# Optimization experiments

Hardware: AMD Instinct MI355X
Metric: run time of the kernel (lower is better)

The kernel has to match this reference:

```python
import jax, jax.numpy as jnp
import numpy as np

N_HEADS = 8
D_K = 64
SCALE = D_K ** (-0.5)


def setup_inputs() -> dict:
    key = jax.random.key(0)
    k1, k2, k3 = jax.random.split(key, 3)
    B, C, H, W = 8, 512, 32, 32
    x = jax.random.normal(k1, (B, C, H, W), dtype=jnp.float32)
    # Linear weights stored as [in, out] so y = x @ W + b (same math as torch Linear)
    W_qkv = jax.random.normal(k2, (C, N_HEADS * D_K * 3), dtype=jnp.float32) * (1.0 / np.sqrt(C))
    b_qkv = jnp.zeros((N_HEADS * D_K * 3,), dtype=jnp.float32)
    W_out = jax.random.normal(k3, (N_HEADS * D_K, C), dtype=jnp.float32) * (1.0 / np.sqrt(N_HEADS * D_K))
    b_out = jnp.zeros((C,), dtype=jnp.float32)
    return {"x": x, "W_qkv": W_qkv, "b_qkv": b_qkv, "W_out": W_out, "b_out": b_out}


def reference(x, W_qkv, b_qkv, W_out, b_out):
    B, C, H, W = x.shape
    N = H * W
    # [B, C, H, W] -> [B, N, C]  (tokens are spatial positions)
    xf = jnp.transpose(x.reshape(B, C, N), (0, 2, 1))
    # NOTE: the original forward never applies self.norm, so neither do we.
    qkv = xf @ W_qkv + b_qkv                       # [B, N, 3*h*d]
    qkv = qkv.reshape(B, N, N_HEADS, 3 * D_K)
    q, k, v = jnp.split(qkv, 3, axis=-1)           # each [B, N, h, d]
    attn = jnp.einsum('bihd,bjhd->bijh', q, k) * SCALE
    attn = jax.nn.softmax(attn, axis=2)            # softmax over key index j
    res = jnp.einsum('bijh,bjhd->bihd', attn, v)   # [B, N, h, d]
    res = res.reshape(B, N, N_HEADS * D_K)
    res = res @ W_out + b_out
    res = res + xf                                 # residual
    res = jnp.transpose(res, (0, 2, 1)).reshape(B, C, H, W)
    return res
```

## Files before the change

kernel.cpp:

```cpp
#include <hip/hip_runtime.h>
#include <hip/hip_bf16.h>
#include <cstdint>

typedef __bf16 bf16;
typedef __attribute__((ext_vector_type(8))) __bf16 bf16x8;
typedef __attribute__((ext_vector_type(4))) __bf16 bf16x4;
typedef __attribute__((ext_vector_type(4))) float f32x4;

#define CEXP 0.1803368801111244f

__global__ __launch_bounds__(256) void prep_all(const float* __restrict__ x,
                                                const float* __restrict__ Wqkv,
                                                const float* __restrict__ Wout,
                                                bf16* __restrict__ xT,
                                                bf16* __restrict__ WqkvT,
                                                bf16* __restrict__ WoutT) {
  __shared__ bf16 t[32][33];
  const int z = blockIdx.z;
  const float* src;
  bf16* dst;
  int C;
  if (z < 8) {
    if (blockIdx.x >= 32) return;
    src = x + (size_t)z * 512 * 1024;
    dst = xT + (size_t)z * 1024 * 512;
    C = 1024;
  } else if (z == 8) {
    src = Wqkv; dst = WqkvT; C = 1536;
  } else {
    if (blockIdx.x >= 16) return;
    src = Wout; dst = WoutT; C = 512;
  }
  const int c0 = blockIdx.x * 32, r0 = blockIdx.y * 32;
  const int tx = threadIdx.x, ty = threadIdx.y;
#pragma unroll
  for (int i = 0; i < 4; ++i)
    t[ty + i * 8][tx] = (bf16)src[(size_t)(r0 + ty + i * 8) * C + c0 + tx];
  __syncthreads();
#pragma unroll
  for (int i = 0; i < 4; ++i)
    dst[(size_t)(c0 + ty + i * 8) * 512 + r0 + tx] = t[tx][ty + i * 8];
}

__global__ __launch_bounds__(256, 3) void gemm_qkv(const bf16* __restrict__ xT,
                                                   const bf16* __restrict__ WqkvT,
                                                   const float* __restrict__ bqkv,
                                                   bf16* __restrict__ Qb,
                                                   bf16* __restrict__ Kb,
                                                   bf16* __restrict__ Vb) {
  __shared__ bf16 As[128 * 72];
  __shared__ bf16 Bs[64 * 72];
  const int b = blockIdx.z;
  const int m0 = blockIdx.y * 128;
  const int co0 = blockIdx.x * 64;
  const int tid = threadIdx.x;
  const int w = tid >> 6, l = tid & 63;
  const int wr = w >> 1, wc = w & 1;
  const int quad = l >> 4, l16 = l & 15;

  const bf16* A = xT + (size_t)b * 1024 * 512;

  f32x4 acc[4][2];
#pragma unroll
  for (int i = 0; i < 4; ++i)
#pragma unroll
    for (int j = 0; j < 2; ++j) acc[i][j] = (f32x4){0.f, 0.f, 0.f, 0.f};

  const int srow = w * 32 + (l >> 3);
  const int scol = (l & 7) * 8;
  const int brow = tid >> 2;
  const int bcol = (tid & 3) * 16;

  for (int kk = 0; kk < 8; ++kk) {
    const int k0 = kk * 64;
    bf16x8 av[4], bv[2];
#pragma unroll
    for (int i = 0; i < 4; ++i)
      av[i] = *(const bf16x8*)&A[(size_t)(m0 + srow + i * 8) * 512 + k0 + scol];
#pragma unroll
    for (int i = 0; i < 2; ++i)
      bv[i] = *(const bf16x8*)&WqkvT[(size_t)(co0 + brow) * 512 + k0 + bcol + i * 8];
#pragma unroll
    for (int i = 0; i < 4; ++i)
      *(bf16x8*)&As[(srow + i * 8) * 72 + scol] = av[i];
#pragma unroll
    for (int i = 0; i < 2; ++i)
      *(bf16x8*)&Bs[brow * 72 + bcol + i * 8] = bv[i];
    __syncthreads();
#pragma unroll
    for (int ks = 0; ks < 2; ++ks) {
      bf16x8 a[4], bb[2];
#pragma unroll
      for (int rb = 0; rb < 4; ++rb)
        a[rb] = *(const bf16x8*)&As[(wr * 64 + rb * 16 + l16) * 72 + ks * 32 + quad * 8];
#pragma unroll
      for (int cb = 0; cb < 2; ++cb)
        bb[cb] = *(const bf16x8*)&Bs[(wc * 32 + cb * 16 + l16) * 72 + ks * 32 + quad * 8];
#pragma unroll
      for (int rb = 0; rb < 4; ++rb)
#pragma unroll
        for (int cb = 0; cb < 2; ++cb)
          acc[rb][cb] = __builtin_amdgcn_mfma_f32_16x16x32_bf16(a[rb], bb[cb], acc[rb][cb], 0, 0, 0);
    }
    __syncthreads();
  }

  const int h = co0 / 192;
  const int part = (co0 - h * 192) >> 6;
#pragma unroll
  for (int cb = 0; cb < 2; ++cb) {
    const int dd = wc * 32 + cb * 16 + l16;
    const float bias = bqkv[co0 + dd];
    if (part == 2) {
      bf16* base = Vb + ((size_t)(b * 8 + h) * 64 + dd) * 1024;
#pragma unroll
      for (int rb = 0; rb < 4; ++rb) {
        const int n = m0 + wr * 64 + rb * 16 + quad * 4;
        f32x4 v = acc[rb][cb];
        bf16x4 ov;
#pragma unroll
        for (int r = 0; r < 4; ++r) ov[r] = (bf16)(v[r] + bias);
        *(bf16x4*)&base[n] = ov;
      }
    } else {
      const float sc = (part == 0) ? CEXP : 1.0f;
      bf16* dst = (part == 0) ? Qb : Kb;
      bf16* base = dst + ((size_t)(b * 8 + h) * 1024) * 64 + dd;
#pragma unroll
      for (int rb = 0; rb < 4; ++rb) {
        const int n = m0 + wr * 64 + rb * 16 + quad * 4;
        f32x4 v = acc[rb][cb];
#pragma unroll
        for (int r = 0; r < 4; ++r) base[(size_t)(n + r) * 64] = (bf16)((v[r] + bias) * sc);
      }
    }
  }
}

__global__ __launch_bounds__(256) void attn_k(const bf16* __restrict__ Qb,
                                              const bf16* __restrict__ Kb,
                                              const bf16* __restrict__ Vb,
                                              bf16* __restrict__ Ob) {
  __shared__ bf16 Ks[128 * 72];
  __shared__ bf16 Vs[64 * 136];
  const int bh = blockIdx.x;
  const int b = bh >> 3, h = bh & 7;
  const int q0 = blockIdx.y * 128;
  const int tid = threadIdx.x;
  const int w = tid >> 6, l = tid & 63;
  const int quad = l >> 4, l16 = l & 15;

  const bf16* Qg = Qb + (size_t)bh * 1024 * 64;
  const bf16* Kg = Kb + (size_t)bh * 1024 * 64;
  const bf16* Vg = Vb + (size_t)bh * 64 * 1024;

  bf16x8 qb[2][2];
#pragma unroll
  for (int mt = 0; mt < 2; ++mt)
#pragma unroll
    for (int ks = 0; ks < 2; ++ks)
      qb[mt][ks] = *(const bf16x8*)&Qg[(size_t)(q0 + w * 32 + mt * 16 + l16) * 64 + ks * 32 + quad * 8];

  bf16x8 ones;
#pragma unroll
  for (int e = 0; e < 8; ++e) ones[e] = (bf16)1.0f;

  f32x4 o[2][4], acc_l[2];
#pragma unroll
  for (int mt = 0; mt < 2; ++mt) {
    acc_l[mt] = (f32x4){0.f, 0.f, 0.f, 0.f};
#pragma unroll
    for (int db = 0; db < 4; ++db) o[mt][db] = (f32x4){0.f, 0.f, 0.f, 0.f};
  }

  const int kr = tid >> 1, kc = (tid & 1) * 32;
  const int vr = tid >> 2, vc = (tid & 3) * 32;

  bf16x8 ka[4], va[4];
#pragma unroll
  for (int e = 0; e < 4; ++e) {
    ka[e] = *(const bf16x8*)&Kg[(size_t)kr * 64 + kc + e * 8];
    va[e] = *(const bf16x8*)&Vg[(size_t)vr * 1024 + vc + e * 8];
  }

  for (int kv = 0; kv < 8; ++kv) {
    __syncthreads();
#pragma unroll
    for (int e = 0; e < 4; ++e) {
      *(bf16x8*)&Ks[kr * 72 + kc + e * 8] = ka[e];
      *(bf16x8*)&Vs[vr * 136 + vc + e * 8] = va[e];
    }
    __syncthreads();
    if (kv < 7) {
      const int j0 = (kv + 1) * 128;
#pragma unroll
      for (int e = 0; e < 4; ++e) {
        ka[e] = *(const bf16x8*)&Kg[(size_t)(j0 + kr) * 64 + kc + e * 8];
        va[e] = *(const bf16x8*)&Vg[(size_t)vr * 1024 + j0 + vc + e * 8];
      }
    }

    f32x4 s[2][8];
#pragma unroll
    for (int mt = 0; mt < 2; ++mt)
#pragma unroll
      for (int jb = 0; jb < 8; ++jb) s[mt][jb] = (f32x4){0.f, 0.f, 0.f, 0.f};
#pragma unroll
    for (int ks = 0; ks < 2; ++ks) {
      bf16x8 kaf[8];
#pragma unroll
      for (int jb = 0; jb < 8; ++jb)
        kaf[jb] = *(const bf16x8*)&Ks[(jb * 16 + l16) * 72 + ks * 32 + quad * 8];
#pragma unroll
      for (int jb = 0; jb < 8; ++jb)
#pragma unroll
        for (int mt = 0; mt < 2; ++mt)
          s[mt][jb] = __builtin_amdgcn_mfma_f32_16x16x32_bf16(kaf[jb], qb[mt][ks], s[mt][jb], 0, 0, 0);
    }

#pragma unroll
    for (int kj = 0; kj < 4; ++kj) {
      bf16x8 bv[4];
#pragma unroll
      for (int db = 0; db < 4; ++db) {
        const bf16x4 lo = *(const bf16x4*)&Vs[(db * 16 + l16) * 136 + kj * 32 + quad * 4];
        const bf16x4 hi = *(const bf16x4*)&Vs[(db * 16 + l16) * 136 + kj * 32 + 16 + quad * 4];
#pragma unroll
        for (int e = 0; e < 4; ++e) {
          bv[db][e] = lo[e];
          bv[db][4 + e] = hi[e];
        }
      }
#pragma unroll
      for (int mt = 0; mt < 2; ++mt) {
        bf16x8 ap;
#pragma unroll
        for (int rr = 0; rr < 4; ++rr) {
          ap[rr] = (bf16)__builtin_amdgcn_exp2f(s[mt][2 * kj][rr]);
          ap[4 + rr] = (bf16)__builtin_amdgcn_exp2f(s[mt][2 * kj + 1][rr]);
        }
        acc_l[mt] = __builtin_amdgcn_mfma_f32_16x16x32_bf16(ap, ones, acc_l[mt], 0, 0, 0);
#pragma unroll
        for (int db = 0; db < 4; ++db)
          o[mt][db] = __builtin_amdgcn_mfma_f32_16x16x32_bf16(ap, bv[db], o[mt][db], 0, 0, 0);
      }
    }
  }

  bf16* Og = Ob + (size_t)b * 1024 * 512 + h * 64;
#pragma unroll
  for (int mt = 0; mt < 2; ++mt) {
    f32x4 inv;
#pragma unroll
    for (int rr = 0; rr < 4; ++rr) inv[rr] = 1.0f / acc_l[mt][rr];
#pragma unroll
    for (int db = 0; db < 4; ++db)
#pragma unroll
      for (int rr = 0; rr < 4; ++rr) {
        const int n = q0 + w * 32 + mt * 16 + quad * 4 + rr;
        Og[(size_t)n * 512 + db * 16 + l16] = (bf16)(o[mt][db][rr] * inv[rr]);
      }
  }
}

__global__ __launch_bounds__(256, 3) void gemm_out(const bf16* __restrict__ Ob,
                                                   const bf16* __restrict__ WoutT,
                                                   const float* __restrict__ bout,
                                                   const float* __restrict__ x,
                                                   float* __restrict__ out) {
  __shared__ bf16 As[128 * 72];
  __shared__ bf16 Bs[64 * 72];
  const int b = blockIdx.z;
  const int m0 = blockIdx.y * 128;
  const int co0 = blockIdx.x * 64;
  const int tid = threadIdx.x;
  const int w = tid >> 6, l = tid & 63;
  const int wr = w >> 1, wc = w & 1;
  const int quad = l >> 4, l16 = l & 15;

  const bf16* A = Ob + (size_t)b * 1024 * 512;

  f32x4 acc[4][2];
#pragma unroll
  for (int i = 0; i < 4; ++i)
#pragma unroll
    for (int j = 0; j < 2; ++j) acc[i][j] = (f32x4){0.f, 0.f, 0.f, 0.f};

  const int srow = w * 32 + (l >> 3);
  const int scol = (l & 7) * 8;
  const int brow = tid >> 2;
  const int bcol = (tid & 3) * 16;

  for (int kk = 0; kk < 8; ++kk) {
    const int k0 = kk * 64;
    bf16x8 av[4], bv[2];
#pragma unroll
    for (int i = 0; i < 4; ++i)
      av[i] = *(const bf16x8*)&A[(size_t)(m0 + srow + i * 8) * 512 + k0 + scol];
#pragma unroll
    for (int i = 0; i < 2; ++i)
      bv[i] = *(const bf16x8*)&WoutT[(size_t)(co0 + brow) * 512 + k0 + bcol + i * 8];
#pragma unroll
    for (int i = 0; i < 4; ++i)
      *(bf16x8*)&As[(srow + i * 8) * 72 + scol] = av[i];
#pragma unroll
    for (int i = 0; i < 2; ++i)
      *(bf16x8*)&Bs[brow * 72 + bcol + i * 8] = bv[i];
    __syncthreads();
#pragma unroll
    for (int ks = 0; ks < 2; ++ks) {
      bf16x8 a[4], bb[2];
#pragma unroll
      for (int rb = 0; rb < 4; ++rb)
        a[rb] = *(const bf16x8*)&As[(wr * 64 + rb * 16 + l16) * 72 + ks * 32 + quad * 8];
#pragma unroll
      for (int cb = 0; cb < 2; ++cb)
        bb[cb] = *(const bf16x8*)&Bs[(wc * 32 + cb * 16 + l16) * 72 + ks * 32 + quad * 8];
#pragma unroll
      for (int rb = 0; rb < 4; ++rb)
#pragma unroll
        for (int cb = 0; cb < 2; ++cb)
          acc[rb][cb] = __builtin_amdgcn_mfma_f32_16x16x32_bf16(a[rb], bb[cb], acc[rb][cb], 0, 0, 0);
    }
    __syncthreads();
  }

#pragma unroll
  for (int cb = 0; cb < 2; ++cb) {
    const int c = co0 + wc * 32 + cb * 16 + l16;
    const float bias = bout[c];
#pragma unroll
    for (int rb = 0; rb < 4; ++rb) {
      const int n = m0 + wr * 64 + rb * 16 + quad * 4;
      const size_t off = ((size_t)b * 512 + c) * 1024 + n;
      f32x4 res = *(const f32x4*)&x[off];
      f32x4 v = acc[rb][cb];
      f32x4 ov;
#pragma unroll
      for (int r = 0; r < 4; ++r) ov[r] = v[r] + bias + res[r];
      *(f32x4*)&out[off] = ov;
    }
  }
}

extern "C" void kernel_launch(void* const* d_in, const int* in_sizes, int n_in,
                              void* d_out, int out_size, void* d_ws, size_t ws_size,
                              hipStream_t stream) {
  const float* x = (const float*)d_in[0];
  const float* Wqkv = (const float*)d_in[1];
  const float* bqkv = (const float*)d_in[2];
  const float* Wout = (const float*)d_in[3];
  const float* bout = (const float*)d_in[4];
  float* out = (float*)d_out;
  char* ws = (char*)d_ws;

  const size_t MB = 1024 * 1024;
  bf16* xT = (bf16*)(ws);
  bf16* Ob = xT;
  bf16* Qbuf = (bf16*)(ws + 8 * MB);
  bf16* Kbuf = (bf16*)(ws + 16 * MB);
  bf16* Vbuf = (bf16*)(ws + 24 * MB);
  bf16* WqkvT = (bf16*)(ws + 32 * MB);
  bf16* WoutT = (bf16*)(ws + 32 * MB + 1572864);
  if (ws_size < 32 * MB + 1572864 + 524288) return;

  prep_all<<<dim3(48, 16, 10), dim3(32, 8), 0, stream>>>(x, Wqkv, Wout, xT, WqkvT, WoutT);
  gemm_qkv<<<dim3(24, 8, 8), 256, 0, stream>>>(xT, WqkvT, bqkv, Qbuf, Kbuf, Vbuf);
  attn_k<<<dim3(64, 8), 256, 0, stream>>>(Qbuf, Kbuf, Vbuf, Ob);
  gemm_out<<<dim3(8, 8, 8), 256, 0, stream>>>(Ob, WoutT, bout, x, out);
}
```

Baseline: 143.2 us.

## Split attention query tile across 8 waves with 16 rows each

The attention kernel now runs 512 threads (8 waves) per block, and each wave handles 16 query rows instead of 32. The K/V tile loads into shared memory are spread over twice as many threads. This halves the per-wave score and output accumulators, lowering register pressure and raising the number of waves available to hide latency. In exchange, each K/V fragment read from shared memory now feeds fewer MFMAs, roughly doubling LDS read traffic per unit of compute.

```diff
diff --git a/kernel.cpp b/kernel.cpp
--- a/kernel.cpp
+++ b/kernel.cpp
@@ -137,10 +137,10 @@
   }
 }
 
-__global__ __launch_bounds__(256) void attn_k(const bf16* __restrict__ Qb,
-                                              const bf16* __restrict__ Kb,
-                                              const bf16* __restrict__ Vb,
-                                              bf16* __restrict__ Ob) {
+__global__ __launch_bounds__(512, 4) void attn_k(const bf16* __restrict__ Qb,
+                                                 const bf16* __restrict__ Kb,
+                                                 const bf16* __restrict__ Vb,
+                                                 bf16* __restrict__ Ob) {
   __shared__ bf16 Ks[128 * 72];
   __shared__ bf16 Vs[64 * 136];
   const int bh = blockIdx.x;
@@ -154,31 +154,25 @@
   const bf16* Kg = Kb + (size_t)bh * 1024 * 64;
   const bf16* Vg = Vb + (size_t)bh * 64 * 1024;
 
-  bf16x8 qb[2][2];
-#pragma unroll
-  for (int mt = 0; mt < 2; ++mt)
-#pragma unroll
-    for (int ks = 0; ks < 2; ++ks)
-      qb[mt][ks] = *(const bf16x8*)&Qg[(size_t)(q0 + w * 32 + mt * 16 + l16) * 64 + ks * 32 + quad * 8];
+  bf16x8 qb[2];
+#pragma unroll
+  for (int ks = 0; ks < 2; ++ks)
+    qb[ks] = *(const bf16x8*)&Qg[(size_t)(q0 + w * 16 + l16) * 64 + ks * 32 + quad * 8];
 
   bf16x8 ones;
 #pragma unroll
   for (int e = 0; e < 8; ++e) ones[e] = (bf16)1.0f;
 
-  f32x4 o[2][4], acc_l[2];
-#pragma unroll
-  for (int mt = 0; mt < 2; ++mt) {
-    acc_l[mt] = (f32x4){0.f, 0.f, 0.f, 0.f};
-#pragma unroll
-    for (int db = 0; db < 4; ++db) o[mt][db] = (f32x4){0.f, 0.f, 0.f, 0.f};
-  }
-
-  const int kr = tid >> 1, kc = (tid & 1) * 32;
-  const int vr = tid >> 2, vc = (tid & 3) * 32;
-
-  bf16x8 ka[4], va[4];
-#pragma unroll
-  for (int e = 0; e < 4; ++e) {
+  f32x4 o[4], acc_l = (f32x4){0.f, 0.f, 0.f, 0.f};
+#pragma unroll
+  for (int db = 0; db < 4; ++db) o[db] = (f32x4){0.f, 0.f, 0.f, 0.f};
+
+  const int kr = tid >> 2, kc = (tid & 3) * 16;
+  const int vr = tid >> 3, vc = (tid & 7) * 16;
+
+  bf16x8 ka[2], va[2];
+#pragma unroll
+  for (int e = 0; e < 2; ++e) {
     ka[e] = *(const bf16x8*)&Kg[(size_t)kr * 64 + kc + e * 8];
     va[e] = *(const bf16x8*)&Vg[(size_t)vr * 1024 + vc + e * 8];
   }
@@ -186,7 +180,7 @@
   for (int kv = 0; kv < 8; ++kv) {
     __syncthreads();
 #pragma unroll
-    for (int e = 0; e < 4; ++e) {
+    for (int e = 0; e < 2; ++e) {
       *(bf16x8*)&Ks[kr * 72 + kc + e * 8] = ka[e];
       *(bf16x8*)&Vs[vr * 136 + vc + e * 8] = va[e];
     }
@@ -194,17 +188,15 @@
     if (kv < 7) {
       const int j0 = (kv + 1) * 128;
 #pragma unroll
-      for (int e = 0; e < 4; ++e) {
+      for (int e = 0; e < 2; ++e) {
         ka[e] = *(const bf16x8*)&Kg[(size_t)(j0 + kr) * 64 + kc + e * 8];
         va[e] = *(const bf16x8*)&Vg[(size_t)vr * 1024 + j0 + vc + e * 8];
       }
     }
 
-    f32x4 s[2][8];
-#pragma unroll
-    for (int mt = 0; mt < 2; ++mt)
-#pragma unroll
-      for (int jb = 0; jb < 8; ++jb) s[mt][jb] = (f32x4){0.f, 0.f, 0.f, 0.f};
+    f32x4 s[8];
+#pragma unroll
+    for (int jb = 0; jb < 8; ++jb) s[jb] = (f32x4){0.f, 0.f, 0.f, 0.f};
 #pragma unroll
     for (int ks = 0; ks < 2; ++ks) {
       bf16x8 kaf[8];
@@ -213,9 +205,7 @@
         kaf[jb] = *(const bf16x8*)&Ks[(jb * 16 + l16) * 72 + ks * 32 + quad * 8];
 #pragma unroll
       for (int jb = 0; jb < 8; ++jb)
-#pragma unroll
-        for (int mt = 0; mt < 2; ++mt)
-          s[mt][jb] = __builtin_amdgcn_mfma_f32_16x16x32_bf16(kaf[jb], qb[mt][ks], s[mt][jb], 0, 0, 0);
+        s[jb] = __builtin_amdgcn_mfma_f32_16x16x32_bf16(kaf[jb], qb[ks], s[jb], 0, 0, 0);
     }
 
 #pragma unroll
@@ -231,36 +221,30 @@
           bv[db][4 + e] = hi[e];
         }
       }
-#pragma unroll
-      for (int mt = 0; mt < 2; ++mt) {
-        bf16x8 ap;
-#pragma unroll
-        for (int rr = 0; rr < 4; ++rr) {
-          ap[rr] = (bf16)__builtin_amdgcn_exp2f(s[mt][2 * kj][rr]);
-          ap[4 + rr] = (bf16)__builtin_amdgcn_exp2f(s[mt][2 * kj + 1][rr]);
-        }
-        acc_l[mt] = __builtin_amdgcn_mfma_f32_16x16x32_bf16(ap, ones, acc_l[mt], 0, 0, 0);
-#pragma unroll
-        for (int db = 0; db < 4; ++db)
-          o[mt][db] = __builtin_amdgcn_mfma_f32_16x16x32_bf16(ap, bv[db], o[mt][db], 0, 0, 0);
-      }
+      bf16x8 ap;
+#pragma unroll
+      for (int rr = 0; rr < 4; ++rr) {
+        ap[rr] = (bf16)__builtin_amdgcn_exp2f(s[2 * kj][rr]);
+        ap[4 + rr] = (bf16)__builtin_amdgcn_exp2f(s[2 * kj + 1][rr]);
+      }
+      acc_l = __builtin_amdgcn_mfma_f32_16x16x32_bf16(ap, ones, acc_l, 0, 0, 0);
+#pragma unroll
+      for (int db = 0; db < 4; ++db)
+        o[db] = __builtin_amdgcn_mfma_f32_16x16x32_bf16(ap, bv[db], o[db], 0, 0, 0);
     }
   }
 
   bf16* Og = Ob + (size_t)b * 1024 * 512 + h * 64;
-#pragma unroll
-  for (int mt = 0; mt < 2; ++mt) {
-    f32x4 inv;
-#pragma unroll
-    for (int rr = 0; rr < 4; ++rr) inv[rr] = 1.0f / acc_l[mt][rr];
-#pragma unroll
-    for (int db = 0; db < 4; ++db)
-#pragma unroll
-      for (int rr = 0; rr < 4; ++rr) {
-        const int n = q0 + w * 32 + mt * 16 + quad * 4 + rr;
-        Og[(size_t)n * 512 + db * 16 + l16] = (bf16)(o[mt][db][rr] * inv[rr]);
-      }
-  }
+  f32x4 inv;
+#pragma unroll
+  for (int rr = 0; rr < 4; ++rr) inv[rr] = 1.0f / acc_l[rr];
+#pragma unroll
+  for (int db = 0; db < 4; ++db)
+#pragma unroll
+    for (int rr = 0; rr < 4; ++rr) {
+      const int n = q0 + w * 16 + quad * 4 + rr;
+      Og[(size_t)n * 512 + db * 16 + l16] = (bf16)(o[db][rr] * inv[rr]);
+    }
 }
 
 __global__ __launch_bounds__(256, 3) void gemm_out(const bf16* __restrict__ Ob,
@@ -366,6 +350,6 @@
 
   prep_all<<<dim3(48, 16, 10), dim3(32, 8), 0, stream>>>(x, Wqkv, Wout, xT, WqkvT, WoutT);
   gemm_qkv<<<dim3(24, 8, 8), 256, 0, stream>>>(xT, WqkvT, bqkv, Qbuf, Kbuf, Vbuf);
-  attn_k<<<dim3(64, 8), 256, 0, stream>>>(Qbuf, Kbuf, Vbuf, Ob);
+  attn_k<<<dim3(64, 8), 512, 0, stream>>>(Qbuf, Kbuf, Vbuf, Ob);
   gemm_out<<<dim3(8, 8, 8), 256, 0, stream>>>(Ob, WoutT, bout, x, out);
 }
```

After: 148.4 us. 3.6% more time.

## Fuse four kernels into one cooperative persistent kernel with grid syncs

Applied to the files above, without the earlier changes.

Merges the prep, QKV GEMM, attention and output GEMM stages into a single cooperative kernel of 512 blocks that separates the stages with grid-wide barriers. Each stage becomes a device function over a shared-memory buffer, and the QKV stage is persisted so each block handles three tiles. The aim is to remove launch gaps and inter-kernel tail effects. It adds grid.sync costs and reduces the scheduler's flexibility, and it falls back to four separate launches if the cooperative launch fails.

```diff
diff --git a/kernel.cpp b/kernel.cpp
--- a/kernel.cpp
+++ b/kernel.cpp
@@ -1,6 +1,9 @@
 #include <hip/hip_runtime.h>
 #include <hip/hip_bf16.h>
+#include <hip/hip_cooperative_groups.h>
 #include <cstdint>
+
+namespace cg = cooperative_groups;
 
 typedef __bf16 bf16;
 typedef __attribute__((ext_vector_type(8))) __bf16 bf16x8;
@@ -8,52 +11,59 @@
 typedef __attribute__((ext_vector_type(4))) float f32x4;
 
 #define CEXP 0.1803368801111244f
-
-__global__ __launch_bounds__(256) void prep_all(const float* __restrict__ x,
-                                                const float* __restrict__ Wqkv,
-                                                const float* __restrict__ Wout,
-                                                bf16* __restrict__ xT,
-                                                bf16* __restrict__ WqkvT,
-                                                bf16* __restrict__ WoutT) {
-  __shared__ bf16 t[32][33];
-  const int z = blockIdx.z;
-  const float* src;
-  bf16* dst;
-  int C;
-  if (z < 8) {
-    if (blockIdx.x >= 32) return;
-    src = x + (size_t)z * 512 * 1024;
-    dst = xT + (size_t)z * 1024 * 512;
-    C = 1024;
-  } else if (z == 8) {
-    src = Wqkv; dst = WqkvT; C = 1536;
-  } else {
-    if (blockIdx.x >= 16) return;
-    src = Wout; dst = WoutT; C = 512;
-  }
-  const int c0 = blockIdx.x * 32, r0 = blockIdx.y * 32;
-  const int tx = threadIdx.x, ty = threadIdx.y;
-#pragma unroll
-  for (int i = 0; i < 4; ++i)
-    t[ty + i * 8][tx] = (bf16)src[(size_t)(r0 + ty + i * 8) * C + c0 + tx];
-  __syncthreads();
-#pragma unroll
-  for (int i = 0; i < 4; ++i)
-    dst[(size_t)(c0 + ty + i * 8) * 512 + r0 + tx] = t[tx][ty + i * 8];
-}
-
-__global__ __launch_bounds__(256, 3) void gemm_qkv(const bf16* __restrict__ xT,
-                                                   const bf16* __restrict__ WqkvT,
-                                                   const float* __restrict__ bqkv,
-                                                   bf16* __restrict__ Qb,
-                                                   bf16* __restrict__ Kb,
-                                                   bf16* __restrict__ Vb) {
-  __shared__ bf16 As[128 * 72];
-  __shared__ bf16 Bs[64 * 72];
-  const int b = blockIdx.z;
-  const int m0 = blockIdx.y * 128;
-  const int co0 = blockIdx.x * 64;
-  const int tid = threadIdx.x;
+#define SMEM_BYTES 35840
+
+__device__ __forceinline__ void prep_phase(char* smem, int blk, int tid,
+                                           const float* __restrict__ x,
+                                           const float* __restrict__ Wqkv,
+                                           const float* __restrict__ Wout,
+                                           bf16* __restrict__ xT,
+                                           bf16* __restrict__ WqkvT,
+                                           bf16* __restrict__ WoutT) {
+  bf16* t = (bf16*)smem;
+  const int tx = tid & 31, ty = tid >> 5;
+  for (int id = blk; id < 5120; id += 512) {
+    const float* src;
+    bf16* dst;
+    int C, r0, c0;
+    if (id < 4096) {
+      const int b = id >> 9, rem = id & 511;
+      r0 = (rem >> 5) * 32;
+      c0 = (rem & 31) * 32;
+      src = x + (size_t)b * 512 * 1024;
+      dst = xT + (size_t)b * 1024 * 512;
+      C = 1024;
+    } else if (id < 4864) {
+      const int u = id - 4096;
+      r0 = (u / 48) * 32;
+      c0 = (u % 48) * 32;
+      src = Wqkv; dst = WqkvT; C = 1536;
+    } else {
+      const int u = id - 4864;
+      r0 = (u >> 4) * 32;
+      c0 = (u & 15) * 32;
+      src = Wout; dst = WoutT; C = 512;
+    }
+#pragma unroll
+    for (int i = 0; i < 4; ++i)
+      t[(ty + i * 8) * 33 + tx] = (bf16)src[(size_t)(r0 + ty + i * 8) * C + c0 + tx];
+    __syncthreads();
+#pragma unroll
+    for (int i = 0; i < 4; ++i)
+      dst[(size_t)(c0 + ty + i * 8) * 512 + r0 + tx] = t[tx * 33 + ty + i * 8];
+    __syncthreads();
+  }
+}
+
+__device__ __forceinline__ void qkv_tile(char* smem, int tid, int b, int m0, int co0,
+                                         const bf16* __restrict__ xT,
+                                         const bf16* __restrict__ WqkvT,
+                                         const float* __restrict__ bqkv,
+                                         bf16* __restrict__ Qb,
+                                         bf16* __restrict__ Kb,
+                                         bf16* __restrict__ Vb) {
+  bf16* As = (bf16*)smem;
+  bf16* Bs = As + 128 * 72;
   const int w = tid >> 6, l = tid & 63;
   const int wr = w >> 1, wc = w & 1;
   const int quad = l >> 4, l16 = l & 15;
@@ -137,16 +147,14 @@
   }
 }
 
-__global__ __launch_bounds__(256) void attn_k(const bf16* __restrict__ Qb,
-                                              const bf16* __restrict__ Kb,
-                                              const bf16* __restrict__ Vb,
-                                              bf16* __restrict__ Ob) {
-  __shared__ bf16 Ks[128 * 72];
-  __shared__ bf16 Vs[64 * 136];
-  const int bh = blockIdx.x;
+__device__ __forceinline__ void attn_tile(char* smem, int tid, int bh, int q0,
+                                          const bf16* __restrict__ Qb,
+                                          const bf16* __restrict__ Kb,
+                                          const bf16* __restrict__ Vb,
+                                          bf16* __restrict__ Ob) {
+  bf16* Ks = (bf16*)smem;
+  bf16* Vs = Ks + 128 * 72;
   const int b = bh >> 3, h = bh & 7;
-  const int q0 = blockIdx.y * 128;
-  const int tid = threadIdx.x;
   const int w = tid >> 6, l = tid & 63;
   const int quad = l >> 4, l16 = l & 15;
 
@@ -263,17 +271,14 @@
   }
 }
 
-__global__ __launch_bounds__(256, 3) void gemm_out(const bf16* __restrict__ Ob,
-                                                   const bf16* __restrict__ WoutT,
-                                                   const float* __restrict__ bout,
-                                                   const float* __restrict__ x,
-                                                   float* __restrict__ out) {
-  __shared__ bf16 As[128 * 72];
-  __shared__ bf16 Bs[64 * 72];
-  const int b = blockIdx.z;
-  const int m0 = blockIdx.y * 128;
-  const int co0 = blockIdx.x * 64;
-  const int tid = threadIdx.x;
+__device__ __forceinline__ void out_tile(char* smem, int tid, int b, int m0, int co0,
+                                         const bf16* __restrict__ Ob,
+                                         const bf16* __restrict__ WoutT,
+                                         const float* __restrict__ bout,
+                                         const float* __restrict__ x,
+                                         float* __restrict__ out) {
+  bf16* As = (bf16*)smem;
+  bf16* Bs = As + 128 * 72;
   const int w = tid >> 6, l = tid & 63;
   const int wr = w >> 1, wc = w & 1;
   const int quad = l >> 4, l16 = l & 15;
@@ -341,6 +346,67 @@
       *(f32x4*)&out[off] = ov;
     }
   }
+}
+
+__global__ __launch_bounds__(256, 2) void fused_k(const float* __restrict__ x,
+                                                  const float* __restrict__ Wqkv,
+                                                  const float* __restrict__ bqkv,
+                                                  const float* __restrict__ Wout,
+                                                  const float* __restrict__ bout,
+                                                  float* __restrict__ out,
+                                                  bf16* __restrict__ xT,
+                                                  bf16* __restrict__ Qb,
+                                                  bf16* __restrict__ Kb,
+                                                  bf16* __restrict__ Vb,
+                                                  bf16* __restrict__ WqkvT,
+                                                  bf16* __restrict__ WoutT) {
+  __shared__ __align__(16) char smem[SMEM_BYTES];
+  const int blk = blockIdx.x, tid = threadIdx.x;
+  cg::grid_group grid = cg::this_grid();
+
+  prep_phase(smem, blk, tid, x, Wqkv, Wout, xT, WqkvT, WoutT);
+  grid.sync();
+#pragma unroll 1
+  for (int tt = 0; tt < 3; ++tt) {
+    const int id = blk * 3 + tt;
+    qkv_tile(smem, tid, id / 192, ((id / 24) & 7) * 128, (id % 24) * 64,
+             xT, WqkvT, bqkv, Qb, Kb, Vb);
+  }
+  grid.sync();
+  attn_tile(smem, tid, blk & 63, (blk >> 6) * 128, Qb, Kb, Vb, xT );
+  grid.sync();
+  out_tile(smem, tid, blk >> 6, ((blk >> 3) & 7) * 128, (blk & 7) * 64,
+           xT , WoutT, bout, x, out);
+}
+
+__global__ __launch_bounds__(256, 2) void prep_k(const float* x, const float* Wqkv,
+                                                 const float* Wout, bf16* xT,
+                                                 bf16* WqkvT, bf16* WoutT) {
+  __shared__ __align__(16) char smem[SMEM_BYTES];
+  prep_phase(smem, blockIdx.x, threadIdx.x, x, Wqkv, Wout, xT, WqkvT, WoutT);
+}
+__global__ __launch_bounds__(256, 2) void qkv_k(const bf16* xT, const bf16* WqkvT,
+                                                const float* bqkv, bf16* Qb, bf16* Kb,
+                                                bf16* Vb) {
+  __shared__ __align__(16) char smem[SMEM_BYTES];
+#pragma unroll 1
+  for (int tt = 0; tt < 3; ++tt) {
+    const int id = blockIdx.x * 3 + tt;
+    qkv_tile(smem, threadIdx.x, id / 192, ((id / 24) & 7) * 128, (id % 24) * 64,
+             xT, WqkvT, bqkv, Qb, Kb, Vb);
+  }
+}
+__global__ __launch_bounds__(256, 2) void attn_k(const bf16* Qb, const bf16* Kb,
+                                                 const bf16* Vb, bf16* Ob) {
+  __shared__ __align__(16) char smem[SMEM_BYTES];
+  attn_tile(smem, threadIdx.x, blockIdx.x & 63, (blockIdx.x >> 6) * 128, Qb, Kb, Vb, Ob);
+}
+__global__ __launch_bounds__(256, 2) void out_k(const bf16* Ob, const bf16* WoutT,
+                                                const float* bout, const float* x,
+                                                float* out) {
+  __shared__ __align__(16) char smem[SMEM_BYTES];
+  out_tile(smem, threadIdx.x, blockIdx.x >> 6, ((blockIdx.x >> 3) & 7) * 128,
+           (blockIdx.x & 7) * 64, Ob, WoutT, bout, x, out);
 }
 
 extern "C" void kernel_launch(void* const* d_in, const int* in_sizes, int n_in,
@@ -356,7 +422,6 @@
 
   const size_t MB = 1024 * 1024;
   bf16* xT = (bf16*)(ws);
-  bf16* Ob = xT;
   bf16* Qbuf = (bf16*)(ws + 8 * MB);
   bf16* Kbuf = (bf16*)(ws + 16 * MB);
   bf16* Vbuf = (bf16*)(ws + 24 * MB);
@@ -364,8 +429,15 @@
   bf16* WoutT = (bf16*)(ws + 32 * MB + 1572864);
   if (ws_size < 32 * MB + 1572864 + 524288) return;
 
-  prep_all<<<dim3(48, 16, 10), dim3(32, 8), 0, stream>>>(x, Wqkv, Wout, xT, WqkvT, WoutT);
-  gemm_qkv<<<dim3(24, 8, 8), 256, 0, stream>>>(xT, WqkvT, bqkv, Qbuf, Kbuf, Vbuf);
-  attn_k<<<dim3(64, 8), 256, 0, stream>>>(Qbuf, Kbuf, Vbuf, Ob);
-  gemm_out<<<dim3(8, 8, 8), 256, 0, stream>>>(Ob, WoutT, bout, x, out);
-}
+  void* args[] = {(void*)&x,    (void*)&Wqkv, (void*)&bqkv,  (void*)&Wout,
+                  (void*)&bout, (void*)&out,  (void*)&xT,    (void*)&Qbuf,
+                  (void*)&Kbuf, (void*)&Vbuf, (void*)&WqkvT, (void*)&WoutT};
+  hipError_t err = hipLaunchCooperativeKernel((const void*)fused_k, dim3(512),
+                                              dim3(256), args, 0, stream);
+  if (err != hipSuccess) {
+    prep_k<<<dim3(512), 256, 0, stream>>>(x, Wqkv, Wout, xT, WqkvT, WoutT);
+    qkv_k<<<dim3(512), 256, 0, stream>>>(xT, WqkvT, bqkv, Qbuf, Kbuf, Vbuf);
+    attn_k<<<dim3(512), 256, 0, stream>>>(Qbuf, Kbuf, Vbuf, xT);
+    out_k<<<dim3(512), 256, 0, stream>>>(xT, WoutT, bout, x, out);
+  }
+}
```

New measurement: 359.7 us. 2.51x slower.
